# Kernel tuning notes

Hardware: AMD Instinct MI355X
Metric: run time of the kernel (lower is better)

## Reference

```python
import jax, jax.numpy as jnp
import numpy as np

B, T, E, HD = 8, 2048, 1024, 64  # batch, seq (== n_ctx), n_embd, head_dim = n_embd // n_head


def setup_inputs() -> dict:
    key = jax.random.key(0)
    k1, k2, k3, k4 = jax.random.split(key, 4)
    x = jax.random.normal(k1, (B, T, E), dtype=jnp.float32)
    s = E ** -0.5  # Linear-like init scale
    Wq = jax.random.normal(k2, (E, HD), dtype=jnp.float32) * s
    Wk = jax.random.normal(k3, (E, HD), dtype=jnp.float32) * s
    Wv = jax.random.normal(k4, (E, HD), dtype=jnp.float32) * s
    return {"x": x, "Wq": Wq, "Wk": Wk, "Wv": Wv}


def reference(x, Wq, Wk, Wv):
    # q,k,v: [B, T, HD]
    q = jnp.einsum('bte,eh->bth', x, Wq)
    k = jnp.einsum('bte,eh->bth', x, Wk)
    v = jnp.einsum('bte,eh->bth', x, Wv)
    scale = k.shape[-1] ** -0.5
    # scores: [B, T, T]
    alpha = jnp.einsum('bqh,bkh->bqk', q, k) * scale
    causal = jnp.tril(jnp.ones((T, T), dtype=bool))
    alpha = jnp.where(causal, alpha, -jnp.inf)
    alpha = jax.nn.softmax(alpha, axis=-1)
    # dropout with p=0.0 is identity in eval
    h = jnp.einsum('bqk,bkh->bqh', alpha, v)  # [B, T, HD]
    return h
```

## Files before the change

### kernel.cpp

```cpp
#include <hip/hip_runtime.h>
#include <hip/hip_bf16.h>
#include <math.h>

#define BATCH 8
#define T 2048
#define E 1024
#define HD 64
#define BT (BATCH * T)

typedef __bf16 bf16_t;
typedef bf16_t bf16x4 __attribute__((ext_vector_type(4)));
typedef bf16_t bf16x8 __attribute__((ext_vector_type(8)));
typedef float f32x4 __attribute__((ext_vector_type(4)));

#define MFMA(a, b, c) __builtin_amdgcn_mfma_f32_16x16x32_bf16((a), (b), (c), 0, 0, 0)

#define QSCALE (0.125f * 1.44269504088896340736f)


__global__ __launch_bounds__(256) void prep_w(const float* __restrict__ Wq,
                                              const float* __restrict__ Wk,
                                              const float* __restrict__ Wv,
                                              bf16_t* __restrict__ WTt) {
    const int nt  = blockIdx.x >> 3;
    const int kc0 = (blockIdx.x & 7) * 128;
    const int tid = threadIdx.x;
    const int l16 = tid & 15;
    const int k8  = (kc0 >> 3) + (tid >> 4);
    const int n   = nt * 16 + l16;
    const int m   = n >> 6;
    const int col = n & 63;
    const float* W = (m == 0) ? Wq : (m == 1) ? Wk : Wv;
    const float scale = (m == 0) ? QSCALE : 1.0f;
    bf16x8 o;
#pragma unroll
    for (int j = 0; j < 8; j++) {
        o[j] = (bf16_t)(W[(size_t)(k8 * 8 + j) * HD + col] * scale);
    }
    *reinterpret_cast<bf16x8*>(WTt + (size_t)nt * 16384 + k8 * 128 + l16 * 8) = o;
}

__global__ __launch_bounds__(256, 2) void qkv_proj(
    const float* __restrict__ x,
    const bf16_t* __restrict__ WTt,
    bf16_t* __restrict__ qt,
    bf16_t* __restrict__ kt,
    bf16_t* __restrict__ vt)
{
    __shared__ __align__(16) float xlds[16][1024];

    const int tid  = threadIdx.x;
    const int wave = tid >> 6;
    const int lane = tid & 63;
    const int l16  = lane & 15;
    const int quad = lane >> 4;
    const int rowbase0 = blockIdx.x * 16;

    const bf16_t* Bb = WTt + (size_t)(wave * 3) * 16384 + lane * 8;

    f32x4 acc[3] = {};

#pragma unroll
    for (int i = 0; i < 16; i++) {
        const int r  = wave * 4 + (i >> 2);
        const int qq = i & 3;
        const float* gsrc = x + (size_t)(rowbase0 + r) * E + qq * 256 +
                            ((lane ^ (r & 7)) * 4);
        __builtin_amdgcn_global_load_lds(
            (const __attribute__((address_space(1))) unsigned int*)gsrc,
            (__attribute__((address_space(3))) unsigned int*)&xlds[r][qq * 256],
            16, 0, 0);
    }
    __syncthreads();

    for (int kc = 0; kc < E; kc += 64) {
        bf16x8 bf[2][3];
#pragma unroll
        for (int ks = 0; ks < 2; ks++) {
#pragma unroll
            for (int tc = 0; tc < 3; tc++) {
                bf[ks][tc] = *reinterpret_cast<const bf16x8*>(
                    Bb + (size_t)tc * 16384 + (kc + ks * 32) * 16);
            }
        }

        const int rx = l16 & 7;
        const int c0 = (kc >> 2) + quad * 2;
        const f32x4 va0 = *reinterpret_cast<const f32x4*>(&xlds[l16][((c0)     ^ rx) * 4]);
        const f32x4 vb0 = *reinterpret_cast<const f32x4*>(&xlds[l16][((c0 + 1) ^ rx) * 4]);
        const f32x4 va1 = *reinterpret_cast<const f32x4*>(&xlds[l16][((c0 + 8) ^ rx) * 4]);
        const f32x4 vb1 = *reinterpret_cast<const f32x4*>(&xlds[l16][((c0 + 9) ^ rx) * 4]);
        bf16x8 a0, a1;
#pragma unroll
        for (int u = 0; u < 4; u++) {
            a0[u]     = (bf16_t)va0[u];
            a0[4 + u] = (bf16_t)vb0[u];
            a1[u]     = (bf16_t)va1[u];
            a1[4 + u] = (bf16_t)vb1[u];
        }

#pragma unroll
        for (int tc = 0; tc < 3; tc++) acc[tc] = MFMA(a0, bf[0][tc], acc[tc]);
#pragma unroll
        for (int tc = 0; tc < 3; tc++) acc[tc] = MFMA(a1, bf[1][tc], acc[tc]);
    }

    const int rowbase = rowbase0;
#pragma unroll
    for (int tc = 0; tc < 3; tc++) {
        const int n0  = wave * 48 + tc * 16;
        const int m   = n0 >> 6;
        const int tcg = (n0 & 63) >> 4;
        if (m < 2) {
            bf16_t* dst = (m == 0) ? qt : kt;
            const size_t o0 = (size_t)(rowbase >> 4) * 1024 +
                              (size_t)(tcg * 2 + (l16 >> 3)) * 128 + (l16 & 7);
#pragma unroll
            for (int r = 0; r < 4; r++) {
                dst[o0 + (quad * 4 + r) * 8] = (bf16_t)acc[tc][r];
            }
        } else {
            const int b_    = rowbase >> 11;
            const int tbase = rowbase & (T - 1);
            const size_t o0 = (size_t)b_ * 131072 +
                              (size_t)((tbase >> 3) + (quad >> 1)) * 128 +
                              l16 * 8 + (quad & 1) * 4 + (size_t)tcg * 32768;
            bf16x4 pv;
#pragma unroll
            for (int r = 0; r < 4; r++) pv[r] = (bf16_t)acc[tc][r];
            *reinterpret_cast<bf16x4*>(vt + o0) = pv;
        }
    }
}

__global__ __launch_bounds__(512, 2) void attn(
    const bf16_t* __restrict__ qtl,
    const bf16_t* __restrict__ ktl,
    const bf16_t* __restrict__ vtl,
    float* __restrict__ out)
{
    __shared__ __align__(16) bf16_t plds[8][16][40];
    __shared__ float opart[8][16][66];
    __shared__ float lpart[8][16];

    const int wave = threadIdx.x >> 6;
    const int lane = threadIdx.x & 63;
    const int l16  = lane & 15;
    const int quad = lane >> 4;
    const int group = wave >> 2;
    const int kw    = wave & 3;

    const int b  = blockIdx.x >> 6;
    const int pr = blockIdx.x & 63;
    const int qt = group ? (127 - pr) : pr;
    const int rowbase = qt * 16;

    const bf16_t* Qb = qtl + (size_t)((b * T + rowbase) >> 4) * 1024 + lane * 8;
    const bf16_t* Kb = ktl + (size_t)b * T * 64 + lane * 8;
    const bf16_t* Vb = vtl + (size_t)b * 131072 + lane * 8;

    const bf16x8 qf0 = *reinterpret_cast<const bf16x8*>(Qb);
    const bf16x8 qf1 = *reinterpret_cast<const bf16x8*>(Qb + 512);

    f32x4 o[4] = {};
    f32x4 lrun = {};

    const int nch = (rowbase + 47) >> 5;

    int k0 = kw * 32;
    bf16x8 kfa0 = *reinterpret_cast<const bf16x8*>(Kb + k0 * 64);
    bf16x8 kfb0 = *reinterpret_cast<const bf16x8*>(Kb + k0 * 64 + 512);
    bf16x8 kfa1 = *reinterpret_cast<const bf16x8*>(Kb + k0 * 64 + 1024);
    bf16x8 kfb1 = *reinterpret_cast<const bf16x8*>(Kb + k0 * 64 + 1536);
    bf16x8 vf0 = *reinterpret_cast<const bf16x8*>(Vb + k0 * 16);
    bf16x8 vf1 = *reinterpret_cast<const bf16x8*>(Vb + k0 * 16 + 32768);
    bf16x8 vf2 = *reinterpret_cast<const bf16x8*>(Vb + k0 * 16 + 65536);
    bf16x8 vf3 = *reinterpret_cast<const bf16x8*>(Vb + k0 * 16 + 98304);

    for (int c = kw; c < nch; c += 4) {
        k0 = c * 32;
        const int cn = (c + 4 < nch) ? (c + 4) : c;
        const int kn = cn * 32;
        bf16x8 nkfa0 = *reinterpret_cast<const bf16x8*>(Kb + kn * 64);
        bf16x8 nkfb0 = *reinterpret_cast<const bf16x8*>(Kb + kn * 64 + 512);
        bf16x8 nkfa1 = *reinterpret_cast<const bf16x8*>(Kb + kn * 64 + 1024);
        bf16x8 nkfb1 = *reinterpret_cast<const bf16x8*>(Kb + kn * 64 + 1536);
        bf16x8 nvf0 = *reinterpret_cast<const bf16x8*>(Vb + kn * 16);
        bf16x8 nvf1 = *reinterpret_cast<const bf16x8*>(Vb + kn * 16 + 32768);
        bf16x8 nvf2 = *reinterpret_cast<const bf16x8*>(Vb + kn * 16 + 65536);
        bf16x8 nvf3 = *reinterpret_cast<const bf16x8*>(Vb + kn * 16 + 98304);

        f32x4 s_lo = {};
        f32x4 s_hi = {};
        s_lo = MFMA(qf0, kfa0, s_lo);
        s_lo = MFMA(qf1, kfb0, s_lo);
        s_hi = MFMA(qf0, kfa1, s_hi);
        s_hi = MFMA(qf1, kfb1, s_hi);

        if (k0 + 31 > rowbase) {
            const int row = rowbase + quad * 4;
#pragma unroll
            for (int r = 0; r < 4; r++) {
                if (k0 + l16 > row + r)      s_lo[r] = -INFINITY;
                if (k0 + 16 + l16 > row + r) s_hi[r] = -INFINITY;
            }
        }

#pragma unroll
        for (int r = 0; r < 4; r++) {
            const float p0 = exp2f(s_lo[r]);
            const float p1 = exp2f(s_hi[r]);
            lrun[r] += p0 + p1;
            plds[wave][quad * 4 + r][l16]      = (bf16_t)p0;
            plds[wave][quad * 4 + r][16 + l16] = (bf16_t)p1;
        }
        const bf16x8 pf = *reinterpret_cast<const bf16x8*>(&plds[wave][l16][quad * 8]);

        o[0] = MFMA(pf, vf0, o[0]);
        o[1] = MFMA(pf, vf1, o[1]);
        o[2] = MFMA(pf, vf2, o[2]);
        o[3] = MFMA(pf, vf3, o[3]);

        kfa0 = nkfa0; kfb0 = nkfb0; kfa1 = nkfa1; kfb1 = nkfb1;
        vf0 = nvf0; vf1 = nvf1; vf2 = nvf2; vf3 = nvf3;
    }

#pragma unroll
    for (int r = 0; r < 4; r++) {
        float l = lrun[r];
        l += __shfl_xor(l, 1);
        l += __shfl_xor(l, 2);
        l += __shfl_xor(l, 4);
        l += __shfl_xor(l, 8);
        if (l16 == 0) lpart[wave][quad * 4 + r] = l;
#pragma unroll
        for (int nb = 0; nb < 4; nb++) {
            opart[wave][quad * 4 + r][nb * 16 + l16] = o[nb][r];
        }
    }
    __syncthreads();

    const int g    = threadIdx.x >> 8;
    const int gtid = threadIdx.x & 255;
    const int qtg  = g ? (127 - pr) : pr;
    const size_t outbase = (size_t)b * T + qtg * 16;
#pragma unroll
    for (int pass = 0; pass < 4; pass++) {
        const int row = pass * 4 + (gtid >> 6);
        const int col = gtid & 63;
        float osum = 0.f, lsum = 0.f;
#pragma unroll
        for (int w = 0; w < 4; w++) {
            osum += opart[g * 4 + w][row][col];
            lsum += lpart[g * 4 + w][row];
        }
        out[(outbase + row) * HD + col] = osum / lsum;
    }
}

extern "C" void kernel_launch(void* const* d_in, const int* in_sizes, int n_in,
                              void* d_out, int out_size, void* d_ws, size_t ws_size,
                              hipStream_t stream) {
    const float* x  = (const float*)d_in[0];
    const float* Wq = (const float*)d_in[1];
    const float* Wk = (const float*)d_in[2];
    const float* Wv = (const float*)d_in[3];
    float* out = (float*)d_out;

    bf16_t* ws  = (bf16_t*)d_ws;
    bf16_t* WTt = ws;
    bf16_t* qtl = WTt + (size_t)192 * E;
    bf16_t* ktl = qtl + (size_t)BT * HD;
    bf16_t* vtl = ktl + (size_t)BT * HD;

    prep_w<<<96, 256, 0, stream>>>(Wq, Wk, Wv, WTt);
    qkv_proj<<<1024, 256, 0, stream>>>(x, WTt, qtl, ktl, vtl);
    attn<<<512, 512, 0, stream>>>(qtl, ktl, vtl, out);
}
```

Baseline: 124.1 us.

## Tile QKV projection over 64 rows with bf16 LDS staging to reuse weights

The QKV projection block now covers 64 rows with 8 waves instead of 16 rows with 4 waves. Each wave computes two 16-row groups, so every weight fragment loaded from global memory feeds twice as many MFMAs. x is converted from fp32 to bf16 once while being staged into a swizzled LDS tile, which removes per-iteration conversions and halves LDS footprint per row. The grid shrinks to 256 blocks of 512 threads, which lowers parallelism and makes the register-based load-convert-store staging synchronous instead of async global_load_lds.

```diff
diff --git a/kernel.cpp b/kernel.cpp
--- a/kernel.cpp
+++ b/kernel.cpp
@@ -40,95 +40,106 @@
     *reinterpret_cast<bf16x8*>(WTt + (size_t)nt * 16384 + k8 * 128 + l16 * 8) = o;
 }
 
-__global__ __launch_bounds__(256, 2) void qkv_proj(
+__global__ __launch_bounds__(512, 2) void qkv_proj(
     const float* __restrict__ x,
     const bf16_t* __restrict__ WTt,
     bf16_t* __restrict__ qt,
     bf16_t* __restrict__ kt,
     bf16_t* __restrict__ vt)
 {
-    __shared__ __align__(16) float xlds[16][1024];
+    __shared__ __align__(16) bf16_t xb[64][1024];
 
     const int tid  = threadIdx.x;
-    const int wave = tid >> 6;
     const int lane = tid & 63;
     const int l16  = lane & 15;
     const int quad = lane >> 4;
-    const int rowbase0 = blockIdx.x * 16;
-
-    const bf16_t* Bb = WTt + (size_t)(wave * 3) * 16384 + lane * 8;
-
-    f32x4 acc[3] = {};
-
-#pragma unroll
-    for (int i = 0; i < 16; i++) {
-        const int r  = wave * 4 + (i >> 2);
-        const int qq = i & 3;
-        const float* gsrc = x + (size_t)(rowbase0 + r) * E + qq * 256 +
-                            ((lane ^ (r & 7)) * 4);
-        __builtin_amdgcn_global_load_lds(
-            (const __attribute__((address_space(1))) unsigned int*)gsrc,
-            (__attribute__((address_space(3))) unsigned int*)&xlds[r][qq * 256],
-            16, 0, 0);
+    const int wc   = (tid >> 6) & 3;
+    const int wr   = tid >> 8;
+    const int rowbase0 = blockIdx.x * 64;
+
+    {
+        const int r   = tid >> 3;
+        const int s   = tid & 7;
+        const int swz = (r & 7) << 4;
+        const float* gsrc = x + (size_t)(rowbase0 + r) * E + s * 128;
+        char* drow = reinterpret_cast<char*>(&xb[r][0]);
+#pragma unroll
+        for (int half = 0; half < 2; half++) {
+            f32x4 v[16];
+#pragma unroll
+            for (int i = 0; i < 16; i++)
+                v[i] = *reinterpret_cast<const f32x4*>(gsrc + half * 64 + i * 4);
+            __builtin_amdgcn_sched_barrier(0);
+#pragma unroll
+            for (int j = 0; j < 8; j++) {
+                bf16x8 w8;
+#pragma unroll
+                for (int u = 0; u < 4; u++) {
+                    w8[u]     = (bf16_t)v[2 * j][u];
+                    w8[4 + u] = (bf16_t)v[2 * j + 1][u];
+                }
+                const int off = s * 256 + half * 128 + j * 16;
+                *reinterpret_cast<bf16x8*>(drow + (off ^ swz)) = w8;
+            }
+        }
     }
     __syncthreads();
+
+    const bf16_t* Bb = WTt + (size_t)(wc * 3) * 16384 + lane * 8;
+    f32x4 acc[2][3] = {};
 
     for (int kc = 0; kc < E; kc += 64) {
         bf16x8 bf[2][3];
 #pragma unroll
-        for (int ks = 0; ks < 2; ks++) {
-#pragma unroll
-            for (int tc = 0; tc < 3; tc++) {
+        for (int ks = 0; ks < 2; ks++)
+#pragma unroll
+            for (int tc = 0; tc < 3; tc++)
                 bf[ks][tc] = *reinterpret_cast<const bf16x8*>(
                     Bb + (size_t)tc * 16384 + (kc + ks * 32) * 16);
+
+#pragma unroll
+        for (int g = 0; g < 2; g++) {
+            const int row = wr * 32 + g * 16 + l16;
+            const int swz = (row & 7) << 4;
+            const char* rbase = reinterpret_cast<const char*>(&xb[row][0]);
+            const bf16x8 a0 = *reinterpret_cast<const bf16x8*>(
+                rbase + ((kc * 2 + quad * 16) ^ swz));
+            const bf16x8 a1 = *reinterpret_cast<const bf16x8*>(
+                rbase + ((kc * 2 + 64 + quad * 16) ^ swz));
+#pragma unroll
+            for (int tc = 0; tc < 3; tc++) acc[g][tc] = MFMA(a0, bf[0][tc], acc[g][tc]);
+#pragma unroll
+            for (int tc = 0; tc < 3; tc++) acc[g][tc] = MFMA(a1, bf[1][tc], acc[g][tc]);
+        }
+    }
+
+#pragma unroll
+    for (int g = 0; g < 2; g++) {
+        const int rowbase = rowbase0 + wr * 32 + g * 16;
+#pragma unroll
+        for (int tc = 0; tc < 3; tc++) {
+            const int n0  = wc * 48 + tc * 16;
+            const int m   = n0 >> 6;
+            const int tcg = (n0 & 63) >> 4;
+            if (m < 2) {
+                bf16_t* dst = (m == 0) ? qt : kt;
+                const size_t o0 = (size_t)(rowbase >> 4) * 1024 +
+                                  (size_t)(tcg * 2 + (l16 >> 3)) * 128 + (l16 & 7);
+#pragma unroll
+                for (int r = 0; r < 4; r++) {
+                    dst[o0 + (quad * 4 + r) * 8] = (bf16_t)acc[g][tc][r];
+                }
+            } else {
+                const int b_    = rowbase >> 11;
+                const int tbase = rowbase & (T - 1);
+                const size_t o0 = (size_t)b_ * 131072 +
+                                  (size_t)((tbase >> 3) + (quad >> 1)) * 128 +
+                                  l16 * 8 + (quad & 1) * 4 + (size_t)tcg * 32768;
+                bf16x4 pv;
+#pragma unroll
+                for (int r = 0; r < 4; r++) pv[r] = (bf16_t)acc[g][tc][r];
+                *reinterpret_cast<bf16x4*>(vt + o0) = pv;
             }
-        }
-
-        const int rx = l16 & 7;
-        const int c0 = (kc >> 2) + quad * 2;
-        const f32x4 va0 = *reinterpret_cast<const f32x4*>(&xlds[l16][((c0)     ^ rx) * 4]);
-        const f32x4 vb0 = *reinterpret_cast<const f32x4*>(&xlds[l16][((c0 + 1) ^ rx) * 4]);
-        const f32x4 va1 = *reinterpret_cast<const f32x4*>(&xlds[l16][((c0 + 8) ^ rx) * 4]);
-        const f32x4 vb1 = *reinterpret_cast<const f32x4*>(&xlds[l16][((c0 + 9) ^ rx) * 4]);
-        bf16x8 a0, a1;
-#pragma unroll
-        for (int u = 0; u < 4; u++) {
-            a0[u]     = (bf16_t)va0[u];
-            a0[4 + u] = (bf16_t)vb0[u];
-            a1[u]     = (bf16_t)va1[u];
-            a1[4 + u] = (bf16_t)vb1[u];
-        }
-
-#pragma unroll
-        for (int tc = 0; tc < 3; tc++) acc[tc] = MFMA(a0, bf[0][tc], acc[tc]);
-#pragma unroll
-        for (int tc = 0; tc < 3; tc++) acc[tc] = MFMA(a1, bf[1][tc], acc[tc]);
-    }
-
-    const int rowbase = rowbase0;
-#pragma unroll
-    for (int tc = 0; tc < 3; tc++) {
-        const int n0  = wave * 48 + tc * 16;
-        const int m   = n0 >> 6;
-        const int tcg = (n0 & 63) >> 4;
-        if (m < 2) {
-            bf16_t* dst = (m == 0) ? qt : kt;
-            const size_t o0 = (size_t)(rowbase >> 4) * 1024 +
-                              (size_t)(tcg * 2 + (l16 >> 3)) * 128 + (l16 & 7);
-#pragma unroll
-            for (int r = 0; r < 4; r++) {
-                dst[o0 + (quad * 4 + r) * 8] = (bf16_t)acc[tc][r];
-            }
-        } else {
-            const int b_    = rowbase >> 11;
-            const int tbase = rowbase & (T - 1);
-            const size_t o0 = (size_t)b_ * 131072 +
-                              (size_t)((tbase >> 3) + (quad >> 1)) * 128 +
-                              l16 * 8 + (quad & 1) * 4 + (size_t)tcg * 32768;
-            bf16x4 pv;
-#pragma unroll
-            for (int r = 0; r < 4; r++) pv[r] = (bf16_t)acc[tc][r];
-            *reinterpret_cast<bf16x4*>(vt + o0) = pv;
         }
     }
 }
@@ -274,6 +285,6 @@
     bf16_t* vtl = ktl + (size_t)BT * HD;
 
     prep_w<<<96, 256, 0, stream>>>(Wq, Wk, Wv, WTt);
-    qkv_proj<<<1024, 256, 0, stream>>>(x, WTt, qtl, ktl, vtl);
+    qkv_proj<<<256, 512, 0, stream>>>(x, WTt, qtl, ktl, vtl);
     attn<<<512, 512, 0, stream>>>(qtl, ktl, vtl, out);
 }
```

After: 122.9 us. No clear change (-0.9%).
